# Kernel optimization log

Measured on AMD Instinct MI355X. Metric: run time of the kernel, lower is better.

The kernel has to match this reference:

```python
import jax, jax.numpy as jnp
import numpy as np
from jax.scipy.special import logsumexp

EPS = 0.05 ** 2        # geomloss: epsilon = blur ** p, blur=0.05, p=2
N_ITER = 20            # fixed Sinkhorn iterations (log-domain)
MARGIN = 10.0
NEG = -1e9             # log-weight for padded points


def _cost(x, y):
    # x: [..., n, d], y: [..., m, d] -> C[..., n, m] = |x - y|^2 / 2 (geomloss p=2)
    sq = (jnp.sum(x * x, -1)[..., :, None] + jnp.sum(y * y, -1)[..., None, :]
          - 2.0 * jnp.einsum('...nd,...md->...nm', x, y))
    return 0.5 * jnp.maximum(sq, 0.0)


def _ot(C, loga, logb):
    # Entropic OT value via log-domain Sinkhorn. C: [..., n, m];
    # loga broadcastable to [..., n], logb broadcastable to [..., m].
    n, m = C.shape[-2], C.shape[-1]
    f0 = jnp.zeros(C.shape[:-1], C.dtype)
    g0 = jnp.zeros(C.shape[:-2] + (m,), C.dtype)

    def step(carry, _):
        f, g = carry
        f = -EPS * logsumexp(logb[..., None, :] + (g[..., None, :] - C) / EPS, axis=-1)
        g = -EPS * logsumexp(loga[..., :, None] + (f[..., :, None] - C) / EPS, axis=-2)
        return (f, g), None

    (f, g), _ = jax.lax.scan(jax.checkpoint(step), (f0, g0), None, length=N_ITER)
    return jnp.sum(jnp.exp(loga) * f, -1) + jnp.sum(jnp.exp(logb) * g, -1)


def setup_inputs() -> dict:
    key = jax.random.key(0)
    k1, k2, k3, k4, k5 = jax.random.split(key, 5)
    B, L, D, K, R = 128, 128, 300, 10, 50
    anchor = jax.random.normal(k1, (B, L, D), dtype=jnp.float32)
    length_anchor = jax.random.randint(k2, (B,), 16, L + 1, dtype=jnp.int32)
    grade = jax.random.randint(k3, (B,), 0, K, dtype=jnp.int32)
    w = jax.random.uniform(k4, (B, L), dtype=jnp.float32)
    mask = (jnp.arange(L)[None, :] < length_anchor[:, None]).astype(jnp.float32)
    w = w * mask
    weight = w / jnp.sum(w, axis=1, keepdims=True)  # valid weights sum to 1
    t0 = jax.random.normal(k5, (K, R, D), dtype=jnp.float32)
    return {"anchor": anchor, "weight": weight, "t0": t0,
            "length_anchor": length_anchor, "grade": grade, "num_class": K}


def reference(anchor, weight, t0, length_anchor, grade, num_class):
    B, L, D = anchor.shape
    K, R, _ = t0.shape
    mask = jnp.arange(L)[None, :] < length_anchor[:, None]          # [B, L]
    logw = jnp.where(mask, jnp.log(jnp.maximum(weight, 1e-12)), NEG)
    logr = jnp.full((R,), -jnp.log(float(R)), anchor.dtype)          # uniform 1/50

    # --- class-prototype pairwise regularizer: dis = sum_ij S(t0_i, t0_j) ---
    ot_tt = _ot(_cost(t0[:, None], t0[None, :]), logr, logr)         # [K, K]
    self_t = jnp.diagonal(ot_tt)                                     # OT(t_k, t_k)
    dis = jnp.sum(ot_tt) - K * jnp.sum(self_t)                       # debiased sum

    # --- per-sample vs every class: debiased Sinkhorn divergences d[b, k] ---
    ot_ab = _ot(_cost(anchor[:, None], t0[None, :]),                 # [B, K, L, R]
                logw[:, None], logr)                                  # -> [B, K]
    ot_aa = _ot(_cost(anchor, anchor), logw, logw)                   # [B]
    d = ot_ab - 0.5 * (ot_aa[:, None] + self_t[None, :])             # [B, K]

    pos = jnp.take_along_axis(d, grade[:, None].astype(jnp.int32), axis=1)[:, 0]
    # sum over k != grade of relu(pos - d_k + 10) == full sum minus relu(10)=10
    loss = jnp.sum(jax.nn.relu(pos[:, None] - d + MARGIN), axis=1) - MARGIN

    return loss.mean() - dis / 100.0  # flag == 1 branch
```

## Files before the change

### kernel.cpp

```cpp
#include <hip/hip_runtime.h>
#include <math.h>


namespace {
constexpr int NB = 128, NL = 128, ND = 300, NK = 10, NR = 50, NITER = 20;
constexpr float LOG2E   = 1.4426950408889634f;
constexpr float EPS     = 0.0025f;
constexpr float CSCALE  = 0.5f * LOG2E / EPS;
constexpr float VSCALE  = EPS * 0.6931471805599453f;
constexpr float LOG2_50 = 5.6438561897747395f;
constexpr float NEGL2   = -1.442695e9f;
constexpr float SENT    = -3.0e38f;
constexpr int KCH = 10;
constexpr int PIT = 40;
}

typedef __attribute__((ext_vector_type(8))) short bf16x8;
typedef __attribute__((ext_vector_type(4))) float f32x4;

__device__ inline float ex2(float x) { return __builtin_amdgcn_exp2f(x); }
__device__ inline float lg2(float x) { return __builtin_amdgcn_logf(x); }
__device__ inline f32x4 vmax4(f32x4 a, f32x4 b) {
  f32x4 r;
  r[0] = fmaxf(a[0], b[0]); r[1] = fmaxf(a[1], b[1]);
  r[2] = fmaxf(a[2], b[2]); r[3] = fmaxf(a[3], b[3]);
  return r;
}
__device__ inline f32x4 vexp4(f32x4 x) {
  f32x4 r;
  r[0] = ex2(x[0]); r[1] = ex2(x[1]); r[2] = ex2(x[2]); r[3] = ex2(x[3]);
  return r;
}

__device__ inline unsigned short f2bf_rn(float x) {
  unsigned int u = __float_as_uint(x);
  unsigned int r = (u + 0x7fffu + ((u >> 16) & 1u)) >> 16;
  return (unsigned short)r;
}
__device__ inline float bf2f(unsigned short h) {
  return __uint_as_float((unsigned int)h << 16);
}

__global__ void prep_kernel(const float* __restrict__ anchor,
                            const float* __restrict__ weight,
                            const float* __restrict__ t0,
                            const int* __restrict__ len,
                            float* __restrict__ na, float* __restrict__ nt,
                            float* __restrict__ lw2) {
  int wid  = (blockIdx.x * blockDim.x + threadIdx.x) >> 6;
  int lane = threadIdx.x & 63;
  const int nA = NB * NL;
  const int total = nA + NK * NR;
  if (wid >= total) return;
  const float* src = (wid < nA) ? (anchor + (size_t)wid * ND)
                                : (t0 + (size_t)(wid - nA) * ND);
  float s = 0.f;
  for (int d = lane; d < ND; d += 64) { float v = src[d]; s += v * v; }
  #pragma unroll
  for (int off = 32; off; off >>= 1) s += __shfl_xor(s, off);
  if (lane == 0) { if (wid < nA) na[wid] = s; else nt[wid - nA] = s; }
  if (wid < nA && lane == 1) {
    int b = wid >> 7, l = wid & 127;
    float w = weight[wid];
    lw2[wid] = (l < len[b]) ? log2f(fmaxf(w, 1e-12f)) : NEGL2;
  }
}

__device__ inline void stage8(const float* __restrict__ src, bool rowvalid,
                              int kg, short* __restrict__ Hs, short* __restrict__ Ls,
                              int lofs) {
  float xv[8];
  if (rowvalid && kg + 8 <= ND) {
    float4 u = *(const float4*)(src + kg);
    float4 v = *(const float4*)(src + kg + 4);
    xv[0]=u.x; xv[1]=u.y; xv[2]=u.z; xv[3]=u.w;
    xv[4]=v.x; xv[5]=v.y; xv[6]=v.z; xv[7]=v.w;
  } else {
    #pragma unroll
    for (int e = 0; e < 8; ++e)
      xv[e] = (rowvalid && kg + e < ND) ? src[kg + e] : 0.f;
  }
  bf16x8 hv, lv;
  #pragma unroll
  for (int e = 0; e < 8; ++e) {
    unsigned short h = f2bf_rn(xv[e]);
    float hf = bf2f(h);
    unsigned short l = f2bf_rn(xv[e] - hf);
    hv[e] = (short)h; lv[e] = (short)l;
  }
  *(bf16x8*)(Hs + lofs) = hv;
  *(bf16x8*)(Ls + lofs) = lv;
}

__global__ __launch_bounds__(512)
void cost_mfma(const float* __restrict__ X, const float* __restrict__ Y,
               const float* __restrict__ NX, const float* __restrict__ NY,
               float* __restrict__ C, int nX, int nY, int mode) {
  __shared__ __align__(16) short Ah[128 * PIT], Al[128 * PIT];
  __shared__ __align__(16) short Bh[128 * PIT], Bl[128 * PIT];

  const int t = threadIdx.x;
  const int i0 = blockIdx.x * 128, j0 = blockIdx.y * 128;
  const int srow = t >> 2, skq = t & 3, kloc = skq * 8;
  const int lofs = srow * PIT + kloc;
  const bool avalid = (i0 + srow) < nX;
  const bool bvalid = (j0 + srow) < nY;
  const float* aro = X + (size_t)(i0 + srow) * ND;
  const float* bro = Y + (size_t)(j0 + srow) * ND;

  const int lane = t & 63, w = t >> 6;
  const int fr = lane & 15, fo = (lane >> 4) * 8;
  const int aofs = (w * 16 + fr) * PIT + fo;

  f32x4 acc[8];
  #pragma unroll
  for (int cc = 0; cc < 8; ++cc) acc[cc] = (f32x4){0.f, 0.f, 0.f, 0.f};

  for (int c = 0; c < KCH; ++c) {
    int kg = c * 32 + kloc;
    stage8(aro, avalid, kg, Ah, Al, lofs);
    stage8(bro, bvalid, kg, Bh, Bl, lofs);
    __syncthreads();

    bf16x8 ah = *(const bf16x8*)(Ah + aofs);
    bf16x8 al = *(const bf16x8*)(Al + aofs);
    #pragma unroll
    for (int cc = 0; cc < 8; ++cc) {
      int bofs = (cc * 16 + fr) * PIT + fo;
      bf16x8 bh = *(const bf16x8*)(Bh + bofs);
      bf16x8 bl = *(const bf16x8*)(Bl + bofs);
      acc[cc] = __builtin_amdgcn_mfma_f32_16x16x32_bf16(ah, bh, acc[cc], 0, 0, 0);
      acc[cc] = __builtin_amdgcn_mfma_f32_16x16x32_bf16(ah, bl, acc[cc], 0, 0, 0);
      acc[cc] = __builtin_amdgcn_mfma_f32_16x16x32_bf16(al, bh, acc[cc], 0, 0, 0);
    }
    __syncthreads();
  }

  #pragma unroll
  for (int cc = 0; cc < 8; ++cc) {
    int gj = j0 + cc * 16 + fr;
    if (gj >= nY) continue;
    float ny = NY[gj];
    #pragma unroll
    for (int reg = 0; reg < 4; ++reg) {
      int gi = i0 + w * 16 + (lane >> 4) * 4 + reg;
      if (gi >= nX) continue;
      float sq = NX[gi] + ny - 2.f * acc[cc][reg];
      float cv = fmaxf(sq, 0.f) * CSCALE;
      if (mode == 0) {
        int k = gj / 50, jj = gj - k * 50;
        C[((size_t)((gi >> 7) * NK + k)) * (NL * NR) + (gi & 127) * NR + jj] = cv;
      } else {
        int ki = gi / 50, ii = gi - ki * 50;
        int kj = gj / 50, jj = gj - kj * 50;
        C[((size_t)(ki * NK + kj)) * (NR * NR) + ii * NR + jj] = cv;
      }
    }
  }
}

__global__ __launch_bounds__(512)
void cost_mfma_aa(const float* __restrict__ X, const float* __restrict__ NX,
                  float* __restrict__ C) {
  __shared__ __align__(16) short Ah[128 * PIT], Al[128 * PIT];

  const int t = threadIdx.x, b = blockIdx.x;
  const int srow = t >> 2, skq = t & 3, kloc = skq * 8;
  const int lofs = srow * PIT + kloc;
  const float* aro = X + (size_t)(b * NL + srow) * ND;

  const int lane = t & 63, w = t >> 6;
  const int fr = lane & 15, fo = (lane >> 4) * 8;
  const int aofs = (w * 16 + fr) * PIT + fo;

  f32x4 acc[8];
  #pragma unroll
  for (int cc = 0; cc < 8; ++cc) acc[cc] = (f32x4){0.f, 0.f, 0.f, 0.f};

  for (int c = 0; c < KCH; ++c) {
    stage8(aro, true, c * 32 + kloc, Ah, Al, lofs);
    __syncthreads();

    bf16x8 ah = *(const bf16x8*)(Ah + aofs);
    bf16x8 al = *(const bf16x8*)(Al + aofs);
    #pragma unroll
    for (int cc = 0; cc < 8; ++cc) {
      int bofs = (cc * 16 + fr) * PIT + fo;
      bf16x8 bh = *(const bf16x8*)(Ah + bofs);
      bf16x8 bl = *(const bf16x8*)(Al + bofs);
      acc[cc] = __builtin_amdgcn_mfma_f32_16x16x32_bf16(ah, bh, acc[cc], 0, 0, 0);
      acc[cc] = __builtin_amdgcn_mfma_f32_16x16x32_bf16(ah, bl, acc[cc], 0, 0, 0);
      acc[cc] = __builtin_amdgcn_mfma_f32_16x16x32_bf16(al, bh, acc[cc], 0, 0, 0);
    }
    __syncthreads();
  }

  const float* nb = NX + b * NL;
  float* Cb = C + (size_t)b * (NL * NL);
  #pragma unroll
  for (int cc = 0; cc < 8; ++cc) {
    int gj = cc * 16 + fr;
    float ny = nb[gj];
    #pragma unroll
    for (int reg = 0; reg < 4; ++reg) {
      int gi = w * 16 + (lane >> 4) * 4 + reg;
      float sq = nb[gi] + ny - 2.f * acc[cc][reg];
      Cb[(size_t)gi * NL + gj] = fmaxf(sq, 0.f) * CSCALE;
    }
  }
}

__global__ __launch_bounds__(256)
void sinkhorn_abtt(const float* __restrict__ Cab, const float* __restrict__ Ctt,
                   const float* __restrict__ lw2, const float* __restrict__ weight,
                   float* __restrict__ oab, float* __restrict__ ott) {
  __shared__ __align__(16) float smem[444];
  const int t = threadIdx.x;

  if (blockIdx.x < NB * NK) {
    float* g2    = smem;
    float* f2    = smem + 56;
    float* potf2 = smem + 184;
    float* la2s  = smem + 312;
    float* red   = smem + 440;
    int p = blockIdx.x, b = p / NK;
    const float* Cp = Cab + (size_t)p * (NL * NR);
    if (t < NL) la2s[t] = lw2[b * NL + t];
    if (t < NR) g2[t] = 0.f;
    else if (t < 56) g2[t] = SENT;

    const int rf = t >> 1, sf = t & 1;
    f32x4 Crow4[7];
    {
      const float* rp = Cp + rf * NR;
      #pragma unroll
      for (int q = 0; q < 7; ++q)
        #pragma unroll
        for (int e = 0; e < 4; ++e) {
          int col = sf * 28 + q * 4 + e;
          Crow4[q][e] = (col < NR) ? -rp[col] : 0.f;
        }
    }
    const int cc = t >> 2, sc = t & 3;
    f32x4 Ccol4[8];
    if (t < 200) {
      #pragma unroll
      for (int q = 0; q < 8; ++q)
        #pragma unroll
        for (int e = 0; e < 4; ++e)
          Ccol4[q][e] = -Cp[(sc * 32 + q * 4 + e) * NR + cc];
    }
    __syncthreads();

    const f32x4* g4base = (const f32x4*)(g2 + sf * 28);
    const f32x4* f4base = (const f32x4*)(potf2 + sc * 32);

    for (int it = 0; it < NITER; ++it) {
      {
        f32x4 x[7];
        f32x4 m4 = {SENT, SENT, SENT, SENT};
        #pragma unroll
        for (int q = 0; q < 7; ++q) {
          x[q] = g4base[q] + Crow4[q];
          m4 = vmax4(m4, x[q]);
        }
        float mx = fmaxf(fmaxf(m4[0], m4[1]), fmaxf(m4[2], m4[3]));
        mx = fmaxf(mx, __shfl_xor(mx, 1));
        f32x4 s4 = {0.f, 0.f, 0.f, 0.f};
        #pragma unroll
        for (int q = 0; q < 7; ++q) s4 += vexp4(x[q] - mx);
        float s = (s4[0] + s4[1]) + (s4[2] + s4[3]);
        s += __shfl_xor(s, 1);
        if (sf == 0) {
          float fv = LOG2_50 - mx - lg2(s);
          f2[rf] = fv; potf2[rf] = la2s[rf] + fv;
        }
      }
      __syncthreads();
      if (t < 200) {
        f32x4 x[8];
        f32x4 m4 = {SENT, SENT, SENT, SENT};
        #pragma unroll
        for (int q = 0; q < 8; ++q) {
          x[q] = f4base[q] + Ccol4[q];
          m4 = vmax4(m4, x[q]);
        }
        float mx = fmaxf(fmaxf(m4[0], m4[1]), fmaxf(m4[2], m4[3]));
        mx = fmaxf(mx, __shfl_xor(mx, 1));
        mx = fmaxf(mx, __shfl_xor(mx, 2));
        f32x4 s4 = {0.f, 0.f, 0.f, 0.f};
        #pragma unroll
        for (int q = 0; q < 8; ++q) s4 += vexp4(x[q] - mx);
        float s = (s4[0] + s4[1]) + (s4[2] + s4[3]);
        s += __shfl_xor(s, 1);
        s += __shfl_xor(s, 2);
        if (sc == 0) g2[cc] = -(mx + lg2(s));
      }
      __syncthreads();
    }

    float acc = 0.f;
    if (t < NL) acc = weight[b * NL + t] * f2[t];
    else if (t < NL + NR) acc = g2[t - NL] * (1.0f / NR);
    #pragma unroll
    for (int off = 32; off; off >>= 1) acc += __shfl_xor(acc, off);
    if ((t & 63) == 0) red[t >> 6] = acc;
    __syncthreads();
    if (t == 0) oab[p] = VSCALE * (red[0] + red[1] + red[2] + red[3]);

  } else {
    float* f2 = smem;
    float* g2 = smem + 56;
    float* red = smem + 112;
    int p = blockIdx.x - NB * NK;
    const float* Cp = Ctt + (size_t)p * (NR * NR);
    if (t < NR) g2[t] = 0.f;

    const int r = t >> 2, sub = t & 3;
    const bool act = (t < 200);
    float Crowb[13], Ccolb[13];
    if (act) {
      #pragma unroll
      for (int j = 0; j < 13; ++j) {
        int idx = sub + 4 * j;
        Crowb[j] = (idx < NR) ? -Cp[r * NR + idx] : SENT;
        Ccolb[j] = (idx < NR) ? -Cp[idx * NR + r] : SENT;
      }
    }
    __syncthreads();

    for (int it = 0; it < NITER; ++it) {
      if (act) {
        float x[13];
        float m0 = SENT, m1 = SENT;
        #pragma unroll
        for (int j = 0; j < 12; j += 2) {
          x[j]     = g2[sub + 4 * j]       + Crowb[j];
          x[j + 1] = g2[sub + 4 * (j + 1)] + Crowb[j + 1];
          m0 = fmaxf(m0, x[j]); m1 = fmaxf(m1, x[j + 1]);
        }
        { int i0 = sub + 48; x[12] = ((i0 < NR) ? g2[i0] : 0.f) + Crowb[12];
          m0 = fmaxf(m0, x[12]); }
        float mx = fmaxf(m0, m1);
        mx = fmaxf(mx, __shfl_xor(mx, 1));
        mx = fmaxf(mx, __shfl_xor(mx, 2));
        float s0 = 0.f, s1 = 0.f;
        #pragma unroll
        for (int j = 0; j < 12; j += 2) {
          s0 += ex2(x[j] - mx); s1 += ex2(x[j + 1] - mx);
        }
        s0 += ex2(x[12] - mx);
        float s = s0 + s1;
        s += __shfl_xor(s, 1);
        s += __shfl_xor(s, 2);
        if (sub == 0) f2[r] = LOG2_50 - mx - lg2(s);
      }
      __syncthreads();
      if (act) {
        float x[13];
        float m0 = SENT, m1 = SENT;
        #pragma unroll
        for (int j = 0; j < 12; j += 2) {
          x[j]     = f2[sub + 4 * j]       + Ccolb[j];
          x[j + 1] = f2[sub + 4 * (j + 1)] + Ccolb[j + 1];
          m0 = fmaxf(m0, x[j]); m1 = fmaxf(m1, x[j + 1]);
        }
        { int i0 = sub + 48; x[12] = ((i0 < NR) ? f2[i0] : 0.f) + Ccolb[12];
          m0 = fmaxf(m0, x[12]); }
        float mx = fmaxf(m0, m1);
        mx = fmaxf(mx, __shfl_xor(mx, 1));
        mx = fmaxf(mx, __shfl_xor(mx, 2));
        float s0 = 0.f, s1 = 0.f;
        #pragma unroll
        for (int j = 0; j < 12; j += 2) {
          s0 += ex2(x[j] - mx); s1 += ex2(x[j + 1] - mx);
        }
        s0 += ex2(x[12] - mx);
        float s = s0 + s1;
        s += __shfl_xor(s, 1);
        s += __shfl_xor(s, 2);
        if (sub == 0) g2[r] = LOG2_50 - mx - lg2(s);
      }
      __syncthreads();
    }

    float acc = 0.f;
    if (t < NR) acc = f2[t] + g2[t];
    #pragma unroll
    for (int off = 32; off; off >>= 1) acc += __shfl_xor(acc, off);
    if ((t & 63) == 0) red[t >> 6] = acc;
    __syncthreads();
    if (t == 0) ott[p] = VSCALE * (1.0f / NR) * (red[0] + red[1] + red[2] + red[3]);
  }
}

__global__ __launch_bounds__(512)
void sinkhorn_aa(const float* __restrict__ Cg, const float* __restrict__ lw2,
                 const float* __restrict__ weight, float* __restrict__ ot) {
  __shared__ __align__(16) float pF[NL];
  __shared__ __align__(16) float pG[NL];
  __shared__ float red[8];
  int b = blockIdx.x, t = threadIdx.x;
  int r = t >> 2, sub = t & 3;
  const float* Cp = Cg + (size_t)b * (NL * NL) + (size_t)r * NL + sub * 32;
  const float* lp = lw2 + b * NL + sub * 32;
  f32x4 Cr4[8];
  #pragma unroll
  for (int q = 0; q < 8; ++q) {
    float4 cv = *(const float4*)(Cp + q * 4);
    float4 lv = *(const float4*)(lp + q * 4);
    Cr4[q] = (f32x4){lv.x - cv.x, lv.y - cv.y, lv.z - cv.z, lv.w - cv.w};
  }
  if (t < NL) pG[t] = 0.f;
  __syncthreads();

  const f32x4* spG = (const f32x4*)(pG + sub * 32);
  const f32x4* spF = (const f32x4*)(pF + sub * 32);

  for (int it = 0; it < NITER; ++it) {
    {
      f32x4 x[8];
      f32x4 m4 = {SENT, SENT, SENT, SENT};
      #pragma unroll
      for (int q = 0; q < 8; ++q) {
        x[q] = spG[q] + Cr4[q];
        m4 = vmax4(m4, x[q]);
      }
      float mx = fmaxf(fmaxf(m4[0], m4[1]), fmaxf(m4[2], m4[3]));
      mx = fmaxf(mx, __shfl_xor(mx, 1));
      mx = fmaxf(mx, __shfl_xor(mx, 2));
      f32x4 s4 = {0.f, 0.f, 0.f, 0.f};
      #pragma unroll
      for (int q = 0; q < 8; ++q) s4 += vexp4(x[q] - mx);
      float s = (s4[0] + s4[1]) + (s4[2] + s4[3]);
      s += __shfl_xor(s, 1);
      s += __shfl_xor(s, 2);
      if (sub == 0) pF[r] = -(mx + lg2(s));
    }
    __syncthreads();
    {
      f32x4 x[8];
      f32x4 m4 = {SENT, SENT, SENT, SENT};
      #pragma unroll
      for (int q = 0; q < 8; ++q) {
        x[q] = spF[q] + Cr4[q];
        m4 = vmax4(m4, x[q]);
      }
      float mx = fmaxf(fmaxf(m4[0], m4[1]), fmaxf(m4[2], m4[3]));
      mx = fmaxf(mx, __shfl_xor(mx, 1));
      mx = fmaxf(mx, __shfl_xor(mx, 2));
      f32x4 s4 = {0.f, 0.f, 0.f, 0.f};
      #pragma unroll
      for (int q = 0; q < 8; ++q) s4 += vexp4(x[q] - mx);
      float s = (s4[0] + s4[1]) + (s4[2] + s4[3]);
      s += __shfl_xor(s, 1);
      s += __shfl_xor(s, 2);
      if (sub == 0) pG[r] = -(mx + lg2(s));
    }
    __syncthreads();
  }

  float acc = 0.f;
  if (t < NL) acc = weight[b * NL + t] * (pF[t] + pG[t]);
  #pragma unroll
  for (int off = 32; off; off >>= 1) acc += __shfl_xor(acc, off);
  if ((t & 63) == 0) red[t >> 6] = acc;
  __syncthreads();
  if (t == 0) {
    float v = 0.f;
    #pragma unroll
    for (int i = 0; i < 8; ++i) v += red[i];
    ot[b] = VSCALE * v;
  }
}

__global__ void finalize_kernel(const float* __restrict__ oab, const float* __restrict__ oaa,
                                const float* __restrict__ ott, const int* __restrict__ grade,
                                float* __restrict__ out) {
  __shared__ float selft[NK];
  __shared__ float redL[4], redD[4];
  int t = threadIdx.x;
  if (t < NK) selft[t] = ott[t * NK + t];
  __syncthreads();
  float dpart = (t < NK * NK) ? ott[t] : 0.f;
  float lpart = 0.f;
  if (t < NB) {
    int g = grade[t];
    float oa = oaa[t];
    float dpos = oab[t * NK + g] - 0.5f * (oa + selft[g]);
    float s = 0.f;
    #pragma unroll
    for (int k = 0; k < NK; ++k) {
      float dk = oab[t * NK + k] - 0.5f * (oa + selft[k]);
      s += fmaxf(dpos - dk + 10.0f, 0.0f);
    }
    lpart = s - 10.0f;
  }
  #pragma unroll
  for (int off = 32; off; off >>= 1) {
    dpart += __shfl_xor(dpart, off);
    lpart += __shfl_xor(lpart, off);
  }
  if ((t & 63) == 0) { redD[t >> 6] = dpart; redL[t >> 6] = lpart; }
  __syncthreads();
  if (t == 0) {
    float ds = 0.f, ls = 0.f;
    #pragma unroll
    for (int i = 0; i < 4; ++i) { ds += redD[i]; ls += redL[i]; }
    float ss = 0.f;
    #pragma unroll
    for (int k = 0; k < NK; ++k) ss += selft[k];
    float dis = ds - (float)NK * ss;
    out[0] = ls / (float)NB - dis * 0.01f;
  }
}

extern "C" void kernel_launch(void* const* d_in, const int* in_sizes, int n_in,
                              void* d_out, int out_size, void* d_ws, size_t ws_size,
                              hipStream_t stream) {
  (void)in_sizes; (void)n_in; (void)out_size; (void)ws_size;
  const float* anchor = (const float*)d_in[0];
  const float* weight = (const float*)d_in[1];
  const float* t0     = (const float*)d_in[2];
  const int*   len    = (const int*)d_in[3];
  const int*   grade  = (const int*)d_in[4];
  float* out = (float*)d_out;

  float* ws  = (float*)d_ws;
  float* Cab = ws;
  float* Caa = Cab + (size_t)NB * NK * NL * NR;
  float* Ctt = Caa + (size_t)NB * NL * NL;
  float* na  = Ctt + (size_t)NK * NK * NR * NR;
  float* nt  = na + NB * NL;
  float* lw2 = nt + NK * NR;
  float* oab = lw2 + NB * NL;
  float* oaa = oab + NB * NK;
  float* ott = oaa + NB;

  prep_kernel<<<(NB * NL + NK * NR) / 4, 256, 0, stream>>>(anchor, weight, t0, len, na, nt, lw2);
  cost_mfma<<<dim3(128, 4), 512, 0, stream>>>(anchor, t0, na, nt, Cab,
                                              NB * NL, NK * NR, 0);
  cost_mfma<<<dim3(4, 4), 512, 0, stream>>>(t0, t0, nt, nt, Ctt,
                                            NK * NR, NK * NR, 2);
  cost_mfma_aa<<<NB, 512, 0, stream>>>(anchor, na, Caa);

  sinkhorn_abtt<<<NB * NK + NK * NK, 256, 0, stream>>>(Cab, Ctt, lw2, weight, oab, ott);
  sinkhorn_aa<<<NB, 512, 0, stream>>>(Caa, lw2, weight, oaa);
  finalize_kernel<<<1, 256, 0, stream>>>(oab, oaa, ott, grade, out);
}
```

Baseline: 200.7 us.

## Skip padded rows beyond per-sample length in cost and Sinkhorn kernels

Passes the per-sample lengths into the cost-matrix and Sinkhorn kernels so that waves, MFMA tiles and logsumexp chunks covering padded rows (index at or beyond the length) are skipped. The column layout in the Sinkhorn reductions is changed to an interleaved 16-element stride so that whole chunks can be dropped when they fall past the length. This cuts global loads, MFMA work and exp evaluations for short sequences. It adds branches and possible divergence, and correctness relies on padded entries contributing negligibly, which holds because their log-weights are -1e9.

```diff
diff --git a/kernel.cpp b/kernel.cpp
--- a/kernel.cpp
+++ b/kernel.cpp
@@ -95,15 +95,17 @@
 __global__ __launch_bounds__(512)
 void cost_mfma(const float* __restrict__ X, const float* __restrict__ Y,
                const float* __restrict__ NX, const float* __restrict__ NY,
+               const int* __restrict__ len,
                float* __restrict__ C, int nX, int nY, int mode) {
   __shared__ __align__(16) short Ah[128 * PIT], Al[128 * PIT];
   __shared__ __align__(16) short Bh[128 * PIT], Bl[128 * PIT];
 
   const int t = threadIdx.x;
   const int i0 = blockIdx.x * 128, j0 = blockIdx.y * 128;
+  const int Lb = len ? len[blockIdx.x] : (1 << 30);
   const int srow = t >> 2, skq = t & 3, kloc = skq * 8;
   const int lofs = srow * PIT + kloc;
-  const bool avalid = (i0 + srow) < nX;
+  const bool avalid = (i0 + srow) < nX && srow < Lb;
   const bool bvalid = (j0 + srow) < nY;
   const float* aro = X + (size_t)(i0 + srow) * ND;
   const float* bro = Y + (size_t)(j0 + srow) * ND;
@@ -111,6 +113,7 @@
   const int lane = t & 63, w = t >> 6;
   const int fr = lane & 15, fo = (lane >> 4) * 8;
   const int aofs = (w * 16 + fr) * PIT + fo;
+  const bool wact = (w * 16 < Lb);
 
   f32x4 acc[8];
   #pragma unroll
@@ -122,16 +125,18 @@
     stage8(bro, bvalid, kg, Bh, Bl, lofs);
     __syncthreads();
 
-    bf16x8 ah = *(const bf16x8*)(Ah + aofs);
-    bf16x8 al = *(const bf16x8*)(Al + aofs);
-    #pragma unroll
-    for (int cc = 0; cc < 8; ++cc) {
-      int bofs = (cc * 16 + fr) * PIT + fo;
-      bf16x8 bh = *(const bf16x8*)(Bh + bofs);
-      bf16x8 bl = *(const bf16x8*)(Bl + bofs);
-      acc[cc] = __builtin_amdgcn_mfma_f32_16x16x32_bf16(ah, bh, acc[cc], 0, 0, 0);
-      acc[cc] = __builtin_amdgcn_mfma_f32_16x16x32_bf16(ah, bl, acc[cc], 0, 0, 0);
-      acc[cc] = __builtin_amdgcn_mfma_f32_16x16x32_bf16(al, bh, acc[cc], 0, 0, 0);
+    if (wact) {
+      bf16x8 ah = *(const bf16x8*)(Ah + aofs);
+      bf16x8 al = *(const bf16x8*)(Al + aofs);
+      #pragma unroll
+      for (int cc = 0; cc < 8; ++cc) {
+        int bofs = (cc * 16 + fr) * PIT + fo;
+        bf16x8 bh = *(const bf16x8*)(Bh + bofs);
+        bf16x8 bl = *(const bf16x8*)(Bl + bofs);
+        acc[cc] = __builtin_amdgcn_mfma_f32_16x16x32_bf16(ah, bh, acc[cc], 0, 0, 0);
+        acc[cc] = __builtin_amdgcn_mfma_f32_16x16x32_bf16(ah, bl, acc[cc], 0, 0, 0);
+        acc[cc] = __builtin_amdgcn_mfma_f32_16x16x32_bf16(al, bh, acc[cc], 0, 0, 0);
+      }
     }
     __syncthreads();
   }
@@ -161,36 +166,43 @@
 
 __global__ __launch_bounds__(512)
 void cost_mfma_aa(const float* __restrict__ X, const float* __restrict__ NX,
-                  float* __restrict__ C) {
+                  const int* __restrict__ len, float* __restrict__ C) {
   __shared__ __align__(16) short Ah[128 * PIT], Al[128 * PIT];
 
   const int t = threadIdx.x, b = blockIdx.x;
+  const int Lb = len[b];
   const int srow = t >> 2, skq = t & 3, kloc = skq * 8;
   const int lofs = srow * PIT + kloc;
   const float* aro = X + (size_t)(b * NL + srow) * ND;
+  const bool avalid = srow < Lb;
 
   const int lane = t & 63, w = t >> 6;
   const int fr = lane & 15, fo = (lane >> 4) * 8;
   const int aofs = (w * 16 + fr) * PIT + fo;
+  const bool wact = (w * 16 < Lb);
 
   f32x4 acc[8];
   #pragma unroll
   for (int cc = 0; cc < 8; ++cc) acc[cc] = (f32x4){0.f, 0.f, 0.f, 0.f};
 
   for (int c = 0; c < KCH; ++c) {
-    stage8(aro, true, c * 32 + kloc, Ah, Al, lofs);
-    __syncthreads();
-
-    bf16x8 ah = *(const bf16x8*)(Ah + aofs);
-    bf16x8 al = *(const bf16x8*)(Al + aofs);
-    #pragma unroll
-    for (int cc = 0; cc < 8; ++cc) {
-      int bofs = (cc * 16 + fr) * PIT + fo;
-      bf16x8 bh = *(const bf16x8*)(Ah + bofs);
-      bf16x8 bl = *(const bf16x8*)(Al + bofs);
-      acc[cc] = __builtin_amdgcn_mfma_f32_16x16x32_bf16(ah, bh, acc[cc], 0, 0, 0);
-      acc[cc] = __builtin_amdgcn_mfma_f32_16x16x32_bf16(ah, bl, acc[cc], 0, 0, 0);
-      acc[cc] = __builtin_amdgcn_mfma_f32_16x16x32_bf16(al, bh, acc[cc], 0, 0, 0);
+    stage8(aro, avalid, c * 32 + kloc, Ah, Al, lofs);
+    __syncthreads();
+
+    if (wact) {
+      bf16x8 ah = *(const bf16x8*)(Ah + aofs);
+      bf16x8 al = *(const bf16x8*)(Al + aofs);
+      #pragma unroll
+      for (int cc = 0; cc < 8; ++cc) {
+        if (cc * 16 < Lb) {
+          int bofs = (cc * 16 + fr) * PIT + fo;
+          bf16x8 bh = *(const bf16x8*)(Ah + bofs);
+          bf16x8 bl = *(const bf16x8*)(Al + bofs);
+          acc[cc] = __builtin_amdgcn_mfma_f32_16x16x32_bf16(ah, bh, acc[cc], 0, 0, 0);
+          acc[cc] = __builtin_amdgcn_mfma_f32_16x16x32_bf16(ah, bl, acc[cc], 0, 0, 0);
+          acc[cc] = __builtin_amdgcn_mfma_f32_16x16x32_bf16(al, bh, acc[cc], 0, 0, 0);
+        }
+      }
     }
     __syncthreads();
   }
@@ -213,6 +225,7 @@
 __global__ __launch_bounds__(256)
 void sinkhorn_abtt(const float* __restrict__ Cab, const float* __restrict__ Ctt,
                    const float* __restrict__ lw2, const float* __restrict__ weight,
+                   const int* __restrict__ len,
                    float* __restrict__ oab, float* __restrict__ ott) {
   __shared__ __align__(16) float smem[444];
   const int t = threadIdx.x;
@@ -224,14 +237,16 @@
     float* la2s  = smem + 312;
     float* red   = smem + 440;
     int p = blockIdx.x, b = p / NK;
+    const int Lb = len[b];
     const float* Cp = Cab + (size_t)p * (NL * NR);
-    if (t < NL) la2s[t] = lw2[b * NL + t];
+    if (t < NL) { la2s[t] = lw2[b * NL + t]; f2[t] = 0.f; potf2[t] = SENT; }
     if (t < NR) g2[t] = 0.f;
     else if (t < 56) g2[t] = SENT;
 
     const int rf = t >> 1, sf = t & 1;
+    const bool fact = (rf < Lb);
     f32x4 Crow4[7];
-    {
+    if (fact) {
       const float* rp = Cp + rf * NR;
       #pragma unroll
       for (int q = 0; q < 7; ++q)
@@ -245,18 +260,20 @@
     f32x4 Ccol4[8];
     if (t < 200) {
       #pragma unroll
-      for (int q = 0; q < 8; ++q)
-        #pragma unroll
-        for (int e = 0; e < 4; ++e)
-          Ccol4[q][e] = -Cp[(sc * 32 + q * 4 + e) * NR + cc];
+      for (int q = 0; q < 8; ++q) {
+        if (16 * q < Lb) {
+          #pragma unroll
+          for (int e = 0; e < 4; ++e)
+            Ccol4[q][e] = -Cp[(16 * q + 4 * sc + e) * NR + cc];
+        }
+      }
     }
     __syncthreads();
 
     const f32x4* g4base = (const f32x4*)(g2 + sf * 28);
-    const f32x4* f4base = (const f32x4*)(potf2 + sc * 32);
 
     for (int it = 0; it < NITER; ++it) {
-      {
+      if (fact) {
         f32x4 x[7];
         f32x4 m4 = {SENT, SENT, SENT, SENT};
         #pragma unroll
@@ -282,15 +299,19 @@
         f32x4 m4 = {SENT, SENT, SENT, SENT};
         #pragma unroll
         for (int q = 0; q < 8; ++q) {
-          x[q] = f4base[q] + Ccol4[q];
-          m4 = vmax4(m4, x[q]);
+          if (16 * q < Lb) {
+            x[q] = *(const f32x4*)(potf2 + 16 * q + 4 * sc) + Ccol4[q];
+            m4 = vmax4(m4, x[q]);
+          }
         }
         float mx = fmaxf(fmaxf(m4[0], m4[1]), fmaxf(m4[2], m4[3]));
         mx = fmaxf(mx, __shfl_xor(mx, 1));
         mx = fmaxf(mx, __shfl_xor(mx, 2));
         f32x4 s4 = {0.f, 0.f, 0.f, 0.f};
         #pragma unroll
-        for (int q = 0; q < 8; ++q) s4 += vexp4(x[q] - mx);
+        for (int q = 0; q < 8; ++q) {
+          if (16 * q < Lb) s4 += vexp4(x[q] - mx);
+        }
         float s = (s4[0] + s4[1]) + (s4[2] + s4[3]);
         s += __shfl_xor(s, 1);
         s += __shfl_xor(s, 2);
@@ -396,62 +417,75 @@
 
 __global__ __launch_bounds__(512)
 void sinkhorn_aa(const float* __restrict__ Cg, const float* __restrict__ lw2,
-                 const float* __restrict__ weight, float* __restrict__ ot) {
+                 const float* __restrict__ weight, const int* __restrict__ len,
+                 float* __restrict__ ot) {
   __shared__ __align__(16) float pF[NL];
   __shared__ __align__(16) float pG[NL];
   __shared__ float red[8];
   int b = blockIdx.x, t = threadIdx.x;
+  const int Lb = len[b];
   int r = t >> 2, sub = t & 3;
-  const float* Cp = Cg + (size_t)b * (NL * NL) + (size_t)r * NL + sub * 32;
-  const float* lp = lw2 + b * NL + sub * 32;
+  const bool ract = (r < Lb);
+  const float* Cr = Cg + (size_t)b * (NL * NL) + (size_t)r * NL;
+  const float* lp = lw2 + b * NL;
   f32x4 Cr4[8];
-  #pragma unroll
-  for (int q = 0; q < 8; ++q) {
-    float4 cv = *(const float4*)(Cp + q * 4);
-    float4 lv = *(const float4*)(lp + q * 4);
-    Cr4[q] = (f32x4){lv.x - cv.x, lv.y - cv.y, lv.z - cv.z, lv.w - cv.w};
-  }
-  if (t < NL) pG[t] = 0.f;
+  if (ract) {
+    #pragma unroll
+    for (int q = 0; q < 8; ++q) {
+      if (16 * q < Lb) {
+        int c0 = 16 * q + 4 * sub;
+        float4 cv = *(const float4*)(Cr + c0);
+        float4 lv = *(const float4*)(lp + c0);
+        Cr4[q] = (f32x4){lv.x - cv.x, lv.y - cv.y, lv.z - cv.z, lv.w - cv.w};
+      }
+    }
+  }
+  if (t < NL) { pG[t] = 0.f; pF[t] = 0.f; }
   __syncthreads();
 
-  const f32x4* spG = (const f32x4*)(pG + sub * 32);
-  const f32x4* spF = (const f32x4*)(pF + sub * 32);
-
   for (int it = 0; it < NITER; ++it) {
-    {
+    if (ract) {
       f32x4 x[8];
       f32x4 m4 = {SENT, SENT, SENT, SENT};
       #pragma unroll
       for (int q = 0; q < 8; ++q) {
-        x[q] = spG[q] + Cr4[q];
-        m4 = vmax4(m4, x[q]);
+        if (16 * q < Lb) {
+          x[q] = *(const f32x4*)(pG + 16 * q + 4 * sub) + Cr4[q];
+          m4 = vmax4(m4, x[q]);
+        }
       }
       float mx = fmaxf(fmaxf(m4[0], m4[1]), fmaxf(m4[2], m4[3]));
       mx = fmaxf(mx, __shfl_xor(mx, 1));
       mx = fmaxf(mx, __shfl_xor(mx, 2));
       f32x4 s4 = {0.f, 0.f, 0.f, 0.f};
       #pragma unroll
-      for (int q = 0; q < 8; ++q) s4 += vexp4(x[q] - mx);
+      for (int q = 0; q < 8; ++q) {
+        if (16 * q < Lb) s4 += vexp4(x[q] - mx);
+      }
       float s = (s4[0] + s4[1]) + (s4[2] + s4[3]);
       s += __shfl_xor(s, 1);
       s += __shfl_xor(s, 2);
       if (sub == 0) pF[r] = -(mx + lg2(s));
     }
     __syncthreads();
-    {
+    if (ract) {
       f32x4 x[8];
       f32x4 m4 = {SENT, SENT, SENT, SENT};
       #pragma unroll
       for (int q = 0; q < 8; ++q) {
-        x[q] = spF[q] + Cr4[q];
-        m4 = vmax4(m4, x[q]);
+        if (16 * q < Lb) {
+          x[q] = *(const f32x4*)(pF + 16 * q + 4 * sub) + Cr4[q];
+          m4 = vmax4(m4, x[q]);
+        }
       }
       float mx = fmaxf(fmaxf(m4[0], m4[1]), fmaxf(m4[2], m4[3]));
       mx = fmaxf(mx, __shfl_xor(mx, 1));
       mx = fmaxf(mx, __shfl_xor(mx, 2));
       f32x4 s4 = {0.f, 0.f, 0.f, 0.f};
       #pragma unroll
-      for (int q = 0; q < 8; ++q) s4 += vexp4(x[q] - mx);
+      for (int q = 0; q < 8; ++q) {
+        if (16 * q < Lb) s4 += vexp4(x[q] - mx);
+      }
       float s = (s4[0] + s4[1]) + (s4[2] + s4[3]);
       s += __shfl_xor(s, 1);
       s += __shfl_xor(s, 2);
@@ -538,13 +572,13 @@
   float* ott = oaa + NB;
 
   prep_kernel<<<(NB * NL + NK * NR) / 4, 256, 0, stream>>>(anchor, weight, t0, len, na, nt, lw2);
-  cost_mfma<<<dim3(128, 4), 512, 0, stream>>>(anchor, t0, na, nt, Cab,
+  cost_mfma<<<dim3(128, 4), 512, 0, stream>>>(anchor, t0, na, nt, len, Cab,
                                               NB * NL, NK * NR, 0);
-  cost_mfma<<<dim3(4, 4), 512, 0, stream>>>(t0, t0, nt, nt, Ctt,
+  cost_mfma<<<dim3(4, 4), 512, 0, stream>>>(t0, t0, nt, nt, nullptr, Ctt,
                                             NK * NR, NK * NR, 2);
-  cost_mfma_aa<<<NB, 512, 0, stream>>>(anchor, na, Caa);
-
-  sinkhorn_abtt<<<NB * NK + NK * NK, 256, 0, stream>>>(Cab, Ctt, lw2, weight, oab, ott);
-  sinkhorn_aa<<<NB, 512, 0, stream>>>(Caa, lw2, weight, oaa);
+  cost_mfma_aa<<<NB, 512, 0, stream>>>(anchor, na, len, Caa);
+
+  sinkhorn_abtt<<<NB * NK + NK * NK, 256, 0, stream>>>(Cab, Ctt, lw2, weight, len, oab, ott);
+  sinkhorn_aa<<<NB, 512, 0, stream>>>(Caa, lw2, weight, len, oaa);
   finalize_kernel<<<1, 256, 0, stream>>>(oab, oaa, ott, grade, out);
 }
```

Result: slower. 223.2 us (+11.2%).

## Merge cost kernels and Sinkhorn kernels into single launches each

Applied to the files above, without the earlier changes.

The three cost-matrix kernels (anchor-prototype, prototype-prototype, anchor-anchor) are combined into one launch that dispatches on block index, and the two Sinkhorn kernels are likewise merged into one. The aa Sinkhorn path moves from 512 to 256 threads per block, with each row handled by 2 threads holding 64 cost entries in registers. The aim is to remove launch gaps and tail idling between small kernels by letting heterogeneous blocks share the GPU. The cost is higher register pressure in the aa path, and the smaller block gives it less parallelism per batch element.

```diff
diff --git a/kernel.cpp b/kernel.cpp
--- a/kernel.cpp
+++ b/kernel.cpp
@@ -13,6 +13,10 @@
 constexpr float SENT    = -3.0e38f;
 constexpr int KCH = 10;
 constexpr int PIT = 40;
+constexpr int NAB_TILES = 512;
+constexpr int NTT_TILES = 16;
+constexpr int SK_AB = NB * NK;
+constexpr int SK_TT = NK * NK;
 }
 
 typedef __attribute__((ext_vector_type(8))) short bf16x8;
@@ -93,131 +97,132 @@
 }
 
 __global__ __launch_bounds__(512)
-void cost_mfma(const float* __restrict__ X, const float* __restrict__ Y,
-               const float* __restrict__ NX, const float* __restrict__ NY,
-               float* __restrict__ C, int nX, int nY, int mode) {
+void cost_all(const float* __restrict__ anchor, const float* __restrict__ t0,
+              const float* __restrict__ na, const float* __restrict__ nt,
+              float* __restrict__ Cab, float* __restrict__ Ctt,
+              float* __restrict__ Caa) {
   __shared__ __align__(16) short Ah[128 * PIT], Al[128 * PIT];
   __shared__ __align__(16) short Bh[128 * PIT], Bl[128 * PIT];
 
+  const int blk = blockIdx.x;
   const int t = threadIdx.x;
-  const int i0 = blockIdx.x * 128, j0 = blockIdx.y * 128;
+  const int lane = t & 63, w = t >> 6;
+  const int fr = lane & 15, fo = (lane >> 4) * 8;
   const int srow = t >> 2, skq = t & 3, kloc = skq * 8;
   const int lofs = srow * PIT + kloc;
-  const bool avalid = (i0 + srow) < nX;
-  const bool bvalid = (j0 + srow) < nY;
-  const float* aro = X + (size_t)(i0 + srow) * ND;
-  const float* bro = Y + (size_t)(j0 + srow) * ND;
-
-  const int lane = t & 63, w = t >> 6;
-  const int fr = lane & 15, fo = (lane >> 4) * 8;
   const int aofs = (w * 16 + fr) * PIT + fo;
 
   f32x4 acc[8];
   #pragma unroll
   for (int cc = 0; cc < 8; ++cc) acc[cc] = (f32x4){0.f, 0.f, 0.f, 0.f};
 
-  for (int c = 0; c < KCH; ++c) {
-    int kg = c * 32 + kloc;
-    stage8(aro, avalid, kg, Ah, Al, lofs);
-    stage8(bro, bvalid, kg, Bh, Bl, lofs);
-    __syncthreads();
-
-    bf16x8 ah = *(const bf16x8*)(Ah + aofs);
-    bf16x8 al = *(const bf16x8*)(Al + aofs);
+  if (blk < NAB_TILES + NTT_TILES) {
+    const float *X, *Y, *NXp, *NYp; float* C;
+    int nX, nY, mode, i0, j0;
+    if (blk < NAB_TILES) {
+      X = anchor; Y = t0; NXp = na; NYp = nt; C = Cab;
+      nX = NB * NL; nY = NK * NR; mode = 0;
+      i0 = (blk & 127) * 128; j0 = (blk >> 7) * 128;
+    } else {
+      int q = blk - NAB_TILES;
+      X = t0; Y = t0; NXp = nt; NYp = nt; C = Ctt;
+      nX = NK * NR; nY = NK * NR; mode = 2;
+      i0 = (q >> 2) * 128; j0 = (q & 3) * 128;
+    }
+    const bool avalid = (i0 + srow) < nX;
+    const bool bvalid = (j0 + srow) < nY;
+    const float* aro = X + (size_t)(i0 + srow) * ND;
+    const float* bro = Y + (size_t)(j0 + srow) * ND;
+
+    for (int c = 0; c < KCH; ++c) {
+      int kg = c * 32 + kloc;
+      stage8(aro, avalid, kg, Ah, Al, lofs);
+      stage8(bro, bvalid, kg, Bh, Bl, lofs);
+      __syncthreads();
+
+      bf16x8 ah = *(const bf16x8*)(Ah + aofs);
+      bf16x8 al = *(const bf16x8*)(Al + aofs);
+      #pragma unroll
+      for (int cc = 0; cc < 8; ++cc) {
+        int bofs = (cc * 16 + fr) * PIT + fo;
+        bf16x8 bh = *(const bf16x8*)(Bh + bofs);
+        bf16x8 bl = *(const bf16x8*)(Bl + bofs);
+        acc[cc] = __builtin_amdgcn_mfma_f32_16x16x32_bf16(ah, bh, acc[cc], 0, 0, 0);
+        acc[cc] = __builtin_amdgcn_mfma_f32_16x16x32_bf16(ah, bl, acc[cc], 0, 0, 0);
+        acc[cc] = __builtin_amdgcn_mfma_f32_16x16x32_bf16(al, bh, acc[cc], 0, 0, 0);
+      }
+      __syncthreads();
+    }
+
     #pragma unroll
     for (int cc = 0; cc < 8; ++cc) {
-      int bofs = (cc * 16 + fr) * PIT + fo;
-      bf16x8 bh = *(const bf16x8*)(Bh + bofs);
-      bf16x8 bl = *(const bf16x8*)(Bl + bofs);
-      acc[cc] = __builtin_amdgcn_mfma_f32_16x16x32_bf16(ah, bh, acc[cc], 0, 0, 0);
-      acc[cc] = __builtin_amdgcn_mfma_f32_16x16x32_bf16(ah, bl, acc[cc], 0, 0, 0);
-      acc[cc] = __builtin_amdgcn_mfma_f32_16x16x32_bf16(al, bh, acc[cc], 0, 0, 0);
-    }
-    __syncthreads();
-  }
-
-  #pragma unroll
-  for (int cc = 0; cc < 8; ++cc) {
-    int gj = j0 + cc * 16 + fr;
-    if (gj >= nY) continue;
-    float ny = NY[gj];
-    #pragma unroll
-    for (int reg = 0; reg < 4; ++reg) {
-      int gi = i0 + w * 16 + (lane >> 4) * 4 + reg;
-      if (gi >= nX) continue;
-      float sq = NX[gi] + ny - 2.f * acc[cc][reg];
-      float cv = fmaxf(sq, 0.f) * CSCALE;
-      if (mode == 0) {
-        int k = gj / 50, jj = gj - k * 50;
-        C[((size_t)((gi >> 7) * NK + k)) * (NL * NR) + (gi & 127) * NR + jj] = cv;
-      } else {
-        int ki = gi / 50, ii = gi - ki * 50;
-        int kj = gj / 50, jj = gj - kj * 50;
-        C[((size_t)(ki * NK + kj)) * (NR * NR) + ii * NR + jj] = cv;
-      }
-    }
-  }
-}
-
-__global__ __launch_bounds__(512)
-void cost_mfma_aa(const float* __restrict__ X, const float* __restrict__ NX,
-                  float* __restrict__ C) {
-  __shared__ __align__(16) short Ah[128 * PIT], Al[128 * PIT];
-
-  const int t = threadIdx.x, b = blockIdx.x;
-  const int srow = t >> 2, skq = t & 3, kloc = skq * 8;
-  const int lofs = srow * PIT + kloc;
-  const float* aro = X + (size_t)(b * NL + srow) * ND;
-
-  const int lane = t & 63, w = t >> 6;
-  const int fr = lane & 15, fo = (lane >> 4) * 8;
-  const int aofs = (w * 16 + fr) * PIT + fo;
-
-  f32x4 acc[8];
-  #pragma unroll
-  for (int cc = 0; cc < 8; ++cc) acc[cc] = (f32x4){0.f, 0.f, 0.f, 0.f};
-
-  for (int c = 0; c < KCH; ++c) {
-    stage8(aro, true, c * 32 + kloc, Ah, Al, lofs);
-    __syncthreads();
-
-    bf16x8 ah = *(const bf16x8*)(Ah + aofs);
-    bf16x8 al = *(const bf16x8*)(Al + aofs);
+      int gj = j0 + cc * 16 + fr;
+      if (gj >= nY) continue;
+      float ny = NYp[gj];
+      #pragma unroll
+      for (int reg = 0; reg < 4; ++reg) {
+        int gi = i0 + w * 16 + (lane >> 4) * 4 + reg;
+        if (gi >= nX) continue;
+        float sq = NXp[gi] + ny - 2.f * acc[cc][reg];
+        float cv = fmaxf(sq, 0.f) * CSCALE;
+        if (mode == 0) {
+          int k = gj / 50, jj = gj - k * 50;
+          C[((size_t)((gi >> 7) * NK + k)) * (NL * NR) + (gi & 127) * NR + jj] = cv;
+        } else {
+          int ki = gi / 50, ii = gi - ki * 50;
+          int kj = gj / 50, jj = gj - kj * 50;
+          C[((size_t)(ki * NK + kj)) * (NR * NR) + ii * NR + jj] = cv;
+        }
+      }
+    }
+  } else {
+    const int b = blk - (NAB_TILES + NTT_TILES);
+    const float* aro = anchor + (size_t)(b * NL + srow) * ND;
+
+    for (int c = 0; c < KCH; ++c) {
+      stage8(aro, true, c * 32 + kloc, Ah, Al, lofs);
+      __syncthreads();
+
+      bf16x8 ah = *(const bf16x8*)(Ah + aofs);
+      bf16x8 al = *(const bf16x8*)(Al + aofs);
+      #pragma unroll
+      for (int cc = 0; cc < 8; ++cc) {
+        int bofs = (cc * 16 + fr) * PIT + fo;
+        bf16x8 bh = *(const bf16x8*)(Ah + bofs);
+        bf16x8 bl = *(const bf16x8*)(Al + bofs);
+        acc[cc] = __builtin_amdgcn_mfma_f32_16x16x32_bf16(ah, bh, acc[cc], 0, 0, 0);
+        acc[cc] = __builtin_amdgcn_mfma_f32_16x16x32_bf16(ah, bl, acc[cc], 0, 0, 0);
+        acc[cc] = __builtin_amdgcn_mfma_f32_16x16x32_bf16(al, bh, acc[cc], 0, 0, 0);
+      }
+      __syncthreads();
+    }
+
+    const float* nb = na + b * NL;
+    float* Cb = Caa + (size_t)b * (NL * NL);
     #pragma unroll
     for (int cc = 0; cc < 8; ++cc) {
-      int bofs = (cc * 16 + fr) * PIT + fo;
-      bf16x8 bh = *(const bf16x8*)(Ah + bofs);
-      bf16x8 bl = *(const bf16x8*)(Al + bofs);
-      acc[cc] = __builtin_amdgcn_mfma_f32_16x16x32_bf16(ah, bh, acc[cc], 0, 0, 0);
-      acc[cc] = __builtin_amdgcn_mfma_f32_16x16x32_bf16(ah, bl, acc[cc], 0, 0, 0);
-      acc[cc] = __builtin_amdgcn_mfma_f32_16x16x32_bf16(al, bh, acc[cc], 0, 0, 0);
-    }
-    __syncthreads();
-  }
-
-  const float* nb = NX + b * NL;
-  float* Cb = C + (size_t)b * (NL * NL);
-  #pragma unroll
-  for (int cc = 0; cc < 8; ++cc) {
-    int gj = cc * 16 + fr;
-    float ny = nb[gj];
-    #pragma unroll
-    for (int reg = 0; reg < 4; ++reg) {
-      int gi = w * 16 + (lane >> 4) * 4 + reg;
-      float sq = nb[gi] + ny - 2.f * acc[cc][reg];
-      Cb[(size_t)gi * NL + gj] = fmaxf(sq, 0.f) * CSCALE;
+      int gj = cc * 16 + fr;
+      float ny = nb[gj];
+      #pragma unroll
+      for (int reg = 0; reg < 4; ++reg) {
+        int gi = w * 16 + (lane >> 4) * 4 + reg;
+        float sq = nb[gi] + ny - 2.f * acc[cc][reg];
+        Cb[(size_t)gi * NL + gj] = fmaxf(sq, 0.f) * CSCALE;
+      }
     }
   }
 }
 
 __global__ __launch_bounds__(256)
-void sinkhorn_abtt(const float* __restrict__ Cab, const float* __restrict__ Ctt,
-                   const float* __restrict__ lw2, const float* __restrict__ weight,
-                   float* __restrict__ oab, float* __restrict__ ott) {
+void sinkhorn_all(const float* __restrict__ Cab, const float* __restrict__ Ctt,
+                  const float* __restrict__ Caa,
+                  const float* __restrict__ lw2, const float* __restrict__ weight,
+                  float* __restrict__ oab, float* __restrict__ ott,
+                  float* __restrict__ oaa) {
   __shared__ __align__(16) float smem[444];
   const int t = threadIdx.x;
 
-  if (blockIdx.x < NB * NK) {
+  if (blockIdx.x < SK_AB) {
     float* g2    = smem;
     float* f2    = smem + 56;
     float* potf2 = smem + 184;
@@ -308,11 +313,11 @@
     __syncthreads();
     if (t == 0) oab[p] = VSCALE * (red[0] + red[1] + red[2] + red[3]);
 
-  } else {
+  } else if (blockIdx.x < SK_AB + SK_TT) {
     float* f2 = smem;
     float* g2 = smem + 56;
     float* red = smem + 112;
-    int p = blockIdx.x - NB * NK;
+    int p = blockIdx.x - SK_AB;
     const float* Cp = Ctt + (size_t)p * (NR * NR);
     if (t < NR) g2[t] = 0.f;
 
@@ -391,86 +396,68 @@
     if ((t & 63) == 0) red[t >> 6] = acc;
     __syncthreads();
     if (t == 0) ott[p] = VSCALE * (1.0f / NR) * (red[0] + red[1] + red[2] + red[3]);
-  }
-}
-
-__global__ __launch_bounds__(512)
-void sinkhorn_aa(const float* __restrict__ Cg, const float* __restrict__ lw2,
-                 const float* __restrict__ weight, float* __restrict__ ot) {
-  __shared__ __align__(16) float pF[NL];
-  __shared__ __align__(16) float pG[NL];
-  __shared__ float red[8];
-  int b = blockIdx.x, t = threadIdx.x;
-  int r = t >> 2, sub = t & 3;
-  const float* Cp = Cg + (size_t)b * (NL * NL) + (size_t)r * NL + sub * 32;
-  const float* lp = lw2 + b * NL + sub * 32;
-  f32x4 Cr4[8];
-  #pragma unroll
-  for (int q = 0; q < 8; ++q) {
-    float4 cv = *(const float4*)(Cp + q * 4);
-    float4 lv = *(const float4*)(lp + q * 4);
-    Cr4[q] = (f32x4){lv.x - cv.x, lv.y - cv.y, lv.z - cv.z, lv.w - cv.w};
-  }
-  if (t < NL) pG[t] = 0.f;
-  __syncthreads();
-
-  const f32x4* spG = (const f32x4*)(pG + sub * 32);
-  const f32x4* spF = (const f32x4*)(pF + sub * 32);
-
-  for (int it = 0; it < NITER; ++it) {
-    {
-      f32x4 x[8];
-      f32x4 m4 = {SENT, SENT, SENT, SENT};
-      #pragma unroll
-      for (int q = 0; q < 8; ++q) {
-        x[q] = spG[q] + Cr4[q];
-        m4 = vmax4(m4, x[q]);
-      }
-      float mx = fmaxf(fmaxf(m4[0], m4[1]), fmaxf(m4[2], m4[3]));
-      mx = fmaxf(mx, __shfl_xor(mx, 1));
-      mx = fmaxf(mx, __shfl_xor(mx, 2));
-      f32x4 s4 = {0.f, 0.f, 0.f, 0.f};
-      #pragma unroll
-      for (int q = 0; q < 8; ++q) s4 += vexp4(x[q] - mx);
-      float s = (s4[0] + s4[1]) + (s4[2] + s4[3]);
-      s += __shfl_xor(s, 1);
-      s += __shfl_xor(s, 2);
-      if (sub == 0) pF[r] = -(mx + lg2(s));
-    }
+
+  } else {
+    float* pF  = smem;
+    float* pG  = smem + 128;
+    float* red = smem + 256;
+    int b = blockIdx.x - (SK_AB + SK_TT);
+    const int r = t >> 1, sub = t & 1;
+    const float* Cr = Caa + (size_t)b * (NL * NL) + (size_t)r * NL;
+    const float* lp = lw2 + b * NL;
+    f32x4 Cr4[16];
+    #pragma unroll
+    for (int q = 0; q < 16; ++q) {
+      int c0 = q * 8 + sub * 4;
+      float4 cv = *(const float4*)(Cr + c0);
+      float4 lv = *(const float4*)(lp + c0);
+      Cr4[q] = (f32x4){lv.x - cv.x, lv.y - cv.y, lv.z - cv.z, lv.w - cv.w};
+    }
+    if (t < NL) { pG[t] = 0.f; pF[t] = 0.f; }
     __syncthreads();
-    {
-      f32x4 x[8];
-      f32x4 m4 = {SENT, SENT, SENT, SENT};
-      #pragma unroll
-      for (int q = 0; q < 8; ++q) {
-        x[q] = spF[q] + Cr4[q];
-        m4 = vmax4(m4, x[q]);
-      }
-      float mx = fmaxf(fmaxf(m4[0], m4[1]), fmaxf(m4[2], m4[3]));
-      mx = fmaxf(mx, __shfl_xor(mx, 1));
-      mx = fmaxf(mx, __shfl_xor(mx, 2));
-      f32x4 s4 = {0.f, 0.f, 0.f, 0.f};
-      #pragma unroll
-      for (int q = 0; q < 8; ++q) s4 += vexp4(x[q] - mx);
-      float s = (s4[0] + s4[1]) + (s4[2] + s4[3]);
-      s += __shfl_xor(s, 1);
-      s += __shfl_xor(s, 2);
-      if (sub == 0) pG[r] = -(mx + lg2(s));
-    }
+
+    for (int it = 0; it < NITER; ++it) {
+      {
+        f32x4 m4 = {SENT, SENT, SENT, SENT};
+        #pragma unroll
+        for (int q = 0; q < 16; ++q)
+          m4 = vmax4(m4, *(const f32x4*)(pG + q * 8 + sub * 4) + Cr4[q]);
+        float mx = fmaxf(fmaxf(m4[0], m4[1]), fmaxf(m4[2], m4[3]));
+        mx = fmaxf(mx, __shfl_xor(mx, 1));
+        f32x4 s4 = {0.f, 0.f, 0.f, 0.f};
+        #pragma unroll
+        for (int q = 0; q < 16; ++q)
+          s4 += vexp4(*(const f32x4*)(pG + q * 8 + sub * 4) + Cr4[q] - mx);
+        float s = (s4[0] + s4[1]) + (s4[2] + s4[3]);
+        s += __shfl_xor(s, 1);
+        if (sub == 0) pF[r] = -(mx + lg2(s));
+      }
+      __syncthreads();
+      {
+        f32x4 m4 = {SENT, SENT, SENT, SENT};
+        #pragma unroll
+        for (int q = 0; q < 16; ++q)
+          m4 = vmax4(m4, *(const f32x4*)(pF + q * 8 + sub * 4) + Cr4[q]);
+        float mx = fmaxf(fmaxf(m4[0], m4[1]), fmaxf(m4[2], m4[3]));
+        mx = fmaxf(mx, __shfl_xor(mx, 1));
+        f32x4 s4 = {0.f, 0.f, 0.f, 0.f};
+        #pragma unroll
+        for (int q = 0; q < 16; ++q)
+          s4 += vexp4(*(const f32x4*)(pF + q * 8 + sub * 4) + Cr4[q] - mx);
+        float s = (s4[0] + s4[1]) + (s4[2] + s4[3]);
+        s += __shfl_xor(s, 1);
+        if (sub == 0) pG[r] = -(mx + lg2(s));
+      }
+      __syncthreads();
+    }
+
+    float acc = 0.f;
+    if (t < NL) acc = weight[b * NL + t] * (pF[t] + pG[t]);
+    #pragma unroll
+    for (int off = 32; off; off >>= 1) acc += __shfl_xor(acc, off);
+    if ((t & 63) == 0) red[t >> 6] = acc;
     __syncthreads();
-  }
-
-  float acc = 0.f;
-  if (t < NL) acc = weight[b * NL + t] * (pF[t] + pG[t]);
-  #pragma unroll
-  for (int off = 32; off; off >>= 1) acc += __shfl_xor(acc, off);
-  if ((t & 63) == 0) red[t >> 6] = acc;
-  __syncthreads();
-  if (t == 0) {
-    float v = 0.f;
-    #pragma unroll
-    for (int i = 0; i < 8; ++i) v += red[i];
-    ot[b] = VSCALE * v;
+    if (t == 0) oaa[b] = VSCALE * (red[0] + red[1] + red[2] + red[3]);
   }
 }
 
@@ -538,13 +525,9 @@
   float* ott = oaa + NB;
 
   prep_kernel<<<(NB * NL + NK * NR) / 4, 256, 0, stream>>>(anchor, weight, t0, len, na, nt, lw2);
-  cost_mfma<<<dim3(128, 4), 512, 0, stream>>>(anchor, t0, na, nt, Cab,
-                                              NB * NL, NK * NR, 0);
-  cost_mfma<<<dim3(4, 4), 512, 0, stream>>>(t0, t0, nt, nt, Ctt,
-                                            NK * NR, NK * NR, 2);
-  cost_mfma_aa<<<NB, 512, 0, stream>>>(anchor, na, Caa);
-
-  sinkhorn_abtt<<<NB * NK + NK * NK, 256, 0, stream>>>(Cab, Ctt, lw2, weight, oab, ott);
-  sinkhorn_aa<<<NB, 512, 0, stream>>>(Caa, lw2, weight, oaa);
+  cost_all<<<NAB_TILES + NTT_TILES + NB, 512, 0, stream>>>(anchor, t0, na, nt,
+                                                           Cab, Ctt, Caa);
+  sinkhorn_all<<<SK_AB + SK_TT + NB, 256, 0, stream>>>(Cab, Ctt, Caa, lw2, weight,
+                                                       oab, ott, oaa);
   finalize_kernel<<<1, 256, 0, stream>>>(oab, oaa, ott, grade, out);
 }
```

Result: faster. 164.7 us (median of 3 runs) (-17.9%).
